# Kernel tuning notes

Measured on AMD Instinct MI355X. Metric: run time of the kernel, lower is better.

## Reference

```python
import jax, jax.numpy as jnp
import numpy as np

RES = 32  # voxel grid resolution per axis (cfg.MODEL.NEURAL_POINTS.VOXEL_RES)


def upsample_ac(x, s):
    """Bilinear upsample with align_corners=True. x: [B,C,h,w] -> [B,C,h*s,w*s]."""
    if s == 1:
        return x
    B, C, h, w = x.shape
    H, W = h * s, w * s
    ys = jnp.arange(H, dtype=x.dtype) * ((h - 1) / (H - 1))
    xs = jnp.arange(W, dtype=x.dtype) * ((w - 1) / (W - 1))
    y0 = jnp.floor(ys).astype(jnp.int32)
    x0 = jnp.floor(xs).astype(jnp.int32)
    y1 = jnp.minimum(y0 + 1, h - 1)
    x1 = jnp.minimum(x0 + 1, w - 1)
    wy = (ys - y0.astype(x.dtype))[:, None]  # [H,1]
    wx = (xs - x0.astype(x.dtype))[None, :]  # [1,W]
    top = x[:, :, y0, :]
    bot = x[:, :, y1, :]
    a = top[..., x0]; b = top[..., x1]; c = bot[..., x0]; d = bot[..., x1]
    return (a * (1 - wx) + b * wx) * (1 - wy) + (c * (1 - wx) + d * wx) * wy


def vox_closest(pos):
    """construct_vox_points_closest: per occupied voxel, index of point closest to
    the voxel's point centroid. pos: [N,3] -> [RES^3] int32 indices."""
    N = pos.shape[0]
    Vn = RES ** 3
    mn = pos.min(0)
    mx = pos.max(0)
    vsz = (mx - mn) / RES  # obtain_voxel_size_based_grid_res
    coord = jnp.clip(jnp.floor((pos - mn) / vsz).astype(jnp.int32), 0, RES - 1)
    vid = (coord[:, 0] * RES + coord[:, 1]) * RES + coord[:, 2]  # [N]
    cnt = jax.ops.segment_sum(jnp.ones((N,), pos.dtype), vid, Vn)
    cen = jax.ops.segment_sum(pos, vid, Vn) / jnp.maximum(cnt, 1.0)[:, None]
    d = jnp.sum((pos - cen[vid]) ** 2, axis=-1)  # [N] dist^2 to own-voxel centroid
    dmin = jax.ops.segment_min(d, vid, Vn)
    cand = jnp.where(d <= dmin[vid], jnp.arange(N, dtype=jnp.int32), N)
    midx = jax.ops.segment_min(cand, vid, Vn)
    return jnp.where(midx >= N, 0, midx)  # guard (rare) empty voxels


def reference(rgb, f1, f2, f3, points_pos, points_dir, W1, b1, W2, b2, points_mask):
    V, _, H, W = rgb.shape
    N = V * H * W
    C = 59
    # valid_index = where(points_mask == 1) (mask is all ones -> identity gather)
    valid = jnp.nonzero(points_mask[0] == 1, size=N, fill_value=0)[0]
    pos = points_pos[0, valid]          # [N,3]
    pdir = points_dir[0, valid]         # [N,3]
    # project_point_feats: upsample each pyramid level to full res, concat channels
    ups = [upsample_ac(rgb, 1), upsample_ac(f1, 2), upsample_ac(f2, 4), upsample_ac(f3, 8)]
    pif = jnp.concatenate(ups, axis=1)                       # [V,59,H,W]
    pif = jnp.transpose(pif, (0, 2, 3, 1)).reshape(N, C)     # [N,59]
    color = jax.lax.stop_gradient(jnp.transpose(rgb, (0, 2, 3, 1)).reshape(N, 3))
    pif = pif[valid]
    color = color[valid]
    emb = jnp.concatenate([pif, pdir], axis=-1)              # [N,62]
    midx = vox_closest(pos)                                  # [32768]
    sel_emb = emb[midx]
    sel_pos = pos[midx]
    sel_color = color[midx]
    sel_dir = pdir[midx]
    # point_mlp (premlp_init): 62 -> 256 -> 256
    h = jax.nn.relu(sel_emb @ W1 + b1)
    points_embedding = h @ W2 + b2
    return points_embedding, sel_pos, sel_color, sel_dir


def setup_inputs() -> dict:
    key = jax.random.key(0)
    ks = jax.random.split(key, 10)
    V, H, W = 8, 240, 320
    N = V * H * W
    return {
        "rgb": jax.random.uniform(ks[0], (V, 3, H, W), jnp.float32),
        "f1": jax.random.normal(ks[1], (V, 8, H // 2, W // 2), jnp.float32),
        "f2": jax.random.normal(ks[2], (V, 16, H // 4, W // 4), jnp.float32),
        "f3": jax.random.normal(ks[3], (V, 32, H // 8, W // 8), jnp.float32),
        "points_pos": jax.random.uniform(ks[4], (1, N, 3), jnp.float32),
        "points_dir": jax.random.normal(ks[5], (1, N, 3), jnp.float32),
        "W1": jax.random.normal(ks[6], (62, 256), jnp.float32) * 0.05,
        "b1": jnp.zeros((256,), jnp.float32),
        "W2": jax.random.normal(ks[7], (256, 256), jnp.float32) * 0.05,
        "b2": jnp.zeros((256,), jnp.float32),
        "points_mask": jnp.ones((1, N), jnp.int32),
    }
```

## Files before the change

kernel.cpp:

```cpp
#include <hip/hip_runtime.h>
#include <hip/hip_bf16.h>
#include <limits.h>
#include <stddef.h>

#define NPTS   614400
#define RESV   32
#define NVOX   (RESV*RESV*RESV)
#define IMG_H  240
#define IMG_W  320
#define IMG_HW (IMG_H*IMG_W)
#define INF    __builtin_inff()
#define CAP    64
#define SPILLCAP 4096

typedef __attribute__((ext_vector_type(8))) short short8;
typedef __attribute__((ext_vector_type(4))) short s16x4;
typedef __attribute__((ext_vector_type(4))) float f32x4;
typedef float f32x4u __attribute__((ext_vector_type(4), aligned(4)));

__device__ __forceinline__ float fadd_(float a, float b){
#pragma clang fp contract(off)
  return a + b;
}
__device__ __forceinline__ float fsub_(float a, float b){
#pragma clang fp contract(off)
  return a - b;
}
__device__ __forceinline__ float fmul_(float a, float b){
#pragma clang fp contract(off)
  return a * b;
}
__device__ __forceinline__ float fdiv_(float a, float b){
#pragma clang fp contract(off)
  return a / b;
}

__device__ __forceinline__ short f2bf(float x){
  __hip_bfloat16 h = __float2bfloat16(x);
  return *reinterpret_cast<short*>(&h);
}

__global__ void k_prep(int* __restrict__ cnt, int* __restrict__ spillcnt,
                       const float* __restrict__ W1, const float* __restrict__ W2,
                       short* __restrict__ W1t, short* __restrict__ W2t,
                       const float* __restrict__ pos,
                       f32x4* __restrict__ pmin, f32x4* __restrict__ pmax,
                       const float* __restrict__ f1, const float* __restrict__ f2,
                       const float* __restrict__ f3,
                       float* __restrict__ f1t, float* __restrict__ f2t,
                       float* __restrict__ f3t, int tposed){
  int gid = blockIdx.x*blockDim.x + threadIdx.x;
  int stride = gridDim.x*blockDim.x;
  if (gid < NVOX) cnt[gid] = 0;
  if (gid == 0) *spillcnt = 0;
  if (gid < 256*64){
    int n = gid >> 6, k = gid & 63;
    W1t[gid] = (k < 62) ? f2bf(W1[k*256 + n]) : (short)0;
  } else if (gid < 256*64 + 256*256){
    int j = gid - 256*64;
    int n = j >> 8, k = j & 255;
    W2t[j] = f2bf(W2[k*256 + n]);
  }

  if (tposed){
    for (int p = gid; p < 8*19200; p += stride){
      int img = p / 19200, pix = p - img*19200;
      const float* s = f1 + (size_t)img*8*19200 + pix;
      float r[8];
      #pragma unroll
      for (int c = 0; c < 8; c++) r[c] = s[(size_t)c*19200];
      float* d = f1t + (size_t)p*8;
      *(f32x4*)&d[0] = (f32x4){r[0],r[1],r[2],r[3]};
      *(f32x4*)&d[4] = (f32x4){r[4],r[5],r[6],r[7]};
    }
    for (int p = gid; p < 8*4800; p += stride){
      int img = p / 4800, pix = p - img*4800;
      const float* s = f2 + (size_t)img*16*4800 + pix;
      float* d = f2t + (size_t)p*16;
      #pragma unroll
      for (int cq = 0; cq < 4; cq++){
        f32x4 v = { s[(size_t)(4*cq+0)*4800], s[(size_t)(4*cq+1)*4800],
                    s[(size_t)(4*cq+2)*4800], s[(size_t)(4*cq+3)*4800] };
        *(f32x4*)&d[4*cq] = v;
      }
    }
    for (int p = gid; p < 8*1200; p += stride){
      int img = p / 1200, pix = p - img*1200;
      const float* s = f3 + (size_t)img*32*1200 + pix;
      float* d = f3t + (size_t)p*32;
      #pragma unroll
      for (int cq = 0; cq < 8; cq++){
        f32x4 v = { s[(size_t)(4*cq+0)*1200], s[(size_t)(4*cq+1)*1200],
                    s[(size_t)(4*cq+2)*1200], s[(size_t)(4*cq+3)*1200] };
        *(f32x4*)&d[4*cq] = v;
      }
    }
  }

  const f32x4* p4 = (const f32x4*)pos;
  float mn[3] = {  INF,  INF,  INF };
  float mx[3] = { -INF, -INF, -INF };
  for (int t = gid; t < NPTS/4; t += stride){
    f32x4 a = p4[3*t+0], b = p4[3*t+1], c = p4[3*t+2];
    mn[0] = fminf(mn[0], fminf(fminf(a.x, a.w), fminf(b.z, c.y)));
    mx[0] = fmaxf(mx[0], fmaxf(fmaxf(a.x, a.w), fmaxf(b.z, c.y)));
    mn[1] = fminf(mn[1], fminf(fminf(a.y, b.x), fminf(b.w, c.z)));
    mx[1] = fmaxf(mx[1], fmaxf(fmaxf(a.y, b.x), fmaxf(b.w, c.z)));
    mn[2] = fminf(mn[2], fminf(fminf(a.z, b.y), fminf(c.x, c.w)));
    mx[2] = fmaxf(mx[2], fmaxf(fmaxf(a.z, b.y), fmaxf(c.x, c.w)));
  }
  #pragma unroll
  for (int off = 32; off >= 1; off >>= 1){
    #pragma unroll
    for (int c = 0; c < 3; c++){
      mn[c] = fminf(mn[c], __shfl_down(mn[c], off, 64));
      mx[c] = fmaxf(mx[c], __shfl_down(mx[c], off, 64));
    }
  }
  __shared__ float smn[4][3], smx[4][3];
  int lane = threadIdx.x & 63, w = threadIdx.x >> 6;
  if (lane == 0){
    #pragma unroll
    for (int c = 0; c < 3; c++){ smn[w][c] = mn[c]; smx[w][c] = mx[c]; }
  }
  __syncthreads();
  if (threadIdx.x == 0){
    f32x4 a, b;
    a.x = fminf(fminf(smn[0][0], smn[1][0]), fminf(smn[2][0], smn[3][0]));
    a.y = fminf(fminf(smn[0][1], smn[1][1]), fminf(smn[2][1], smn[3][1]));
    a.z = fminf(fminf(smn[0][2], smn[1][2]), fminf(smn[2][2], smn[3][2]));
    a.w = 0.f;
    b.x = fmaxf(fmaxf(smx[0][0], smx[1][0]), fmaxf(smx[2][0], smx[3][0]));
    b.y = fmaxf(fmaxf(smx[0][1], smx[1][1]), fmaxf(smx[2][1], smx[3][1]));
    b.z = fmaxf(fmaxf(smx[0][2], smx[1][2]), fmaxf(smx[2][2], smx[3][2]));
    b.w = 0.f;
    pmin[blockIdx.x] = a;
    pmax[blockIdx.x] = b;
  }
}

__device__ __forceinline__ void reduce_minmax(const f32x4* __restrict__ pmin,
                                              const f32x4* __restrict__ pmax,
                                              float mn[3], float vsz[3]){
  int t = threadIdx.x;
  f32x4 a = pmin[t], b = pmin[t+256];
  f32x4 c = pmax[t], d = pmax[t+256];
  float lmn[3] = { fminf(a.x,b.x), fminf(a.y,b.y), fminf(a.z,b.z) };
  float lmx[3] = { fmaxf(c.x,d.x), fmaxf(c.y,d.y), fmaxf(c.z,d.z) };
  #pragma unroll
  for (int off = 32; off >= 1; off >>= 1){
    #pragma unroll
    for (int k = 0; k < 3; k++){
      lmn[k] = fminf(lmn[k], __shfl_xor(lmn[k], off, 64));
      lmx[k] = fmaxf(lmx[k], __shfl_xor(lmx[k], off, 64));
    }
  }
  __shared__ float smn[4][3], smx[4][3];
  int lane = t & 63, w = t >> 6;
  if (lane == 0){
    #pragma unroll
    for (int k = 0; k < 3; k++){ smn[w][k] = lmn[k]; smx[w][k] = lmx[k]; }
  }
  __syncthreads();
  #pragma unroll
  for (int k = 0; k < 3; k++){
    mn[k] = fminf(fminf(smn[0][k], smn[1][k]), fminf(smn[2][k], smn[3][k]));
    float mx = fmaxf(fmaxf(smx[0][k], smx[1][k]), fmaxf(smx[2][k], smx[3][k]));
    vsz[k] = fdiv_(fsub_(mx, mn[k]), 32.0f);
  }
}

__global__ void k_scatter(const float* __restrict__ pos,
                          const f32x4* __restrict__ pmin, const f32x4* __restrict__ pmax,
                          int* __restrict__ cnt, int* __restrict__ slots,
                          int* __restrict__ spillcnt, int2* __restrict__ spill){
  float mn[3], vsz[3];
  reduce_minmax(pmin, pmax, mn, vsz);

  int t = blockIdx.x*blockDim.x + threadIdx.x;
  const f32x4* p4 = (const f32x4*)pos;
  f32x4 a = p4[3*t+0], b = p4[3*t+1], c = p4[3*t+2];
  float X[4] = {a.x, a.w, b.z, c.y};
  float Y[4] = {a.y, b.x, b.w, c.z};
  float Z[4] = {a.z, b.y, c.x, c.w};
  #pragma unroll
  for (int j = 0; j < 4; j++){
    int i = 4*t + j;
    float P[3] = {X[j], Y[j], Z[j]};
    int v = 0;
    #pragma unroll
    for (int k = 0; k < 3; k++){
      float tt = fdiv_(fsub_(P[k], mn[k]), vsz[k]);
      int cc = (int)floorf(tt);
      cc = min(max(cc, 0), RESV-1);
      v = v*RESV + cc;
    }
    int p = atomicAdd(&cnt[v], 1);
    if (p < CAP){
      slots[v*CAP + p] = i;
    } else {
      int sp = atomicAdd(spillcnt, 1);
      if (sp < SPILLCAP){ int2 e; e.x = v; e.y = i; spill[sp] = e; }
    }
  }
}

__launch_bounds__(256)
__global__ void k_voxfull(const int* __restrict__ cnt, const int* __restrict__ slots,
                          const int* __restrict__ spillcnt, const int2* __restrict__ spill,
                          const float* __restrict__ pos,
                          const float* __restrict__ pdir, const float* __restrict__ rgb,
                          const float* __restrict__ f1, const float* __restrict__ f2,
                          const float* __restrict__ f3,
                          const float* __restrict__ f1t, const float* __restrict__ f2t,
                          const float* __restrict__ f3t, int tposed,
                          float* __restrict__ selpos, float* __restrict__ selcol,
                          float* __restrict__ seldir, short* __restrict__ emb){
  int lane = threadIdx.x & 63;
  int v = blockIdx.x*4 + (threadIdx.x >> 6);
  int n = cnt[v];
  int m = 0;
  unsigned long long ball = 0;
  float px = 0.f, py = 0.f, pz = 0.f;

  if (n > CAP){
    if (lane == 0){
      int sc = min(*spillcnt, SPILLCAP);
      float sx = 0.f, sy = 0.f, sz = 0.f; int last = -1;
      for (int i = 0; i < n; i++){
        int best = INT_MAX;
        for (int j = 0; j < CAP; j++){
          int id = slots[v*CAP + j];
          if (id > last && id < best) best = id;
        }
        for (int j = 0; j < sc; j++){
          int2 e = spill[j];
          if (e.x == v && e.y > last && e.y < best) best = e.y;
        }
        sx = fadd_(sx, pos[3*best+0]);
        sy = fadd_(sy, pos[3*best+1]);
        sz = fadd_(sz, pos[3*best+2]);
        last = best;
      }
      float cf = (float)n;
      float cx = fdiv_(sx, cf), cy = fdiv_(sy, cf), cz = fdiv_(sz, cf);
      float dmin = INF; int mm = 0;
      for (int j = 0; j < CAP + sc; j++){
        int id; int ok = 1;
        if (j < CAP) id = slots[v*CAP + j];
        else { int2 e = spill[j-CAP]; ok = (e.x == v); id = e.y; }
        if (!ok) continue;
        float dx = fsub_(pos[3*id+0], cx);
        float dy = fsub_(pos[3*id+1], cy);
        float dz = fsub_(pos[3*id+2], cz);
        float d  = fadd_(fadd_(fmul_(dx,dx), fmul_(dy,dy)), fmul_(dz,dz));
        if (d < dmin || (d == dmin && id < mm)){ dmin = d; mm = id; }
      }
      m = mm;
    }
    m = __shfl(m, 0, 64);
  } else {
    int key = INT_MAX;
    float gx = 0.f, gy = 0.f, gz = 0.f;
    if (lane < n){
      key = slots[v*CAP + lane];
      if (key < NPTS-1){
        f32x4u q = *(const f32x4u*)&pos[3*key];
        gx = q.x; gy = q.y; gz = q.z;
      } else {
        gx = pos[3*key+0]; gy = pos[3*key+1]; gz = pos[3*key+2];
      }
    }
    int src = lane;
    #pragma unroll
    for (int k = 2; k <= 64; k <<= 1){
      #pragma unroll
      for (int j = k >> 1; j >= 1; j >>= 1){
        int ok = __shfl_xor(key, j, 64);
        int os = __shfl_xor(src, j, 64);
        bool up    = ((lane & k) == 0);
        bool lower = ((lane & j) == 0);
        bool sw = (lower == up) ? (ok < key) : (ok > key);
        if (sw){ key = ok; src = os; }
      }
    }
    px = __shfl(gx, src, 64);
    py = __shfl(gy, src, 64);
    pz = __shfl(gz, src, 64);

    float sx = 0.f, sy = 0.f, sz = 0.f;
    for (int i = 0; i < n; i++){
      sx = fadd_(sx, __shfl(px, i, 64));
      sy = fadd_(sy, __shfl(py, i, 64));
      sz = fadd_(sz, __shfl(pz, i, 64));
    }
    float cf = fmaxf((float)n, 1.0f);
    float cx = fdiv_(sx, cf), cy = fdiv_(sy, cf), cz = fdiv_(sz, cf);

    float bd = INF; int bi = 0;
    if (lane < n){
      float dx = fsub_(px, cx), dy = fsub_(py, cy), dz = fsub_(pz, cz);
      bd = fadd_(fadd_(fmul_(dx,dx), fmul_(dy,dy)), fmul_(dz,dz));
      bi = key;
    }
    #pragma unroll
    for (int off = 32; off >= 1; off >>= 1){
      float od = __shfl_xor(bd, off, 64);
      int   oi = __shfl_xor(bi, off, 64);
      if (od < bd || (od == bd && oi < bi)){ bd = od; bi = oi; }
    }
    m = bi;
    ball = __ballot(lane < n && key == m);
  }

  float wx_ = 0.f, wy_ = 0.f, wz_ = 0.f;
  if (ball){
    int wl = (int)(__ffsll((long long)ball) - 1);
    wx_ = __shfl(px, wl, 64);
    wy_ = __shfl(py, wl, 64);
    wz_ = __shfl(pz, wl, 64);
  }

  int img = m / IMG_HW;
  int rem = m - img*IMG_HW;
  int y = rem / IMG_W;
  int x = rem - y*IMG_W;
  int ch = lane;
  float val;
  if (ch < 3){
    val = rgb[((img*3 + ch)*IMG_H + y)*IMG_W + x];
    selcol[3*v+ch] = val;
    float sp = ball ? ((ch == 0) ? wx_ : (ch == 1) ? wy_ : wz_) : pos[3*m+ch];
    selpos[3*v+ch] = sp;
  } else if (ch < 59){
    int lvl = (ch >= 27) ? 2 : ((ch >= 11) ? 1 : 0);
    int c   = ch - ((lvl == 0) ? 3 : ((lvl == 1) ? 11 : 27));
    int C   = 8 << lvl;
    int h   = 120 >> lvl, w = 160 >> lvl;
    float ry = (lvl == 0) ? (119.0f/239.0f) : ((lvl == 1) ? (59.0f/239.0f) : (29.0f/239.0f));
    float rx = (lvl == 0) ? (159.0f/319.0f) : ((lvl == 1) ? (79.0f/319.0f) : (39.0f/319.0f));
    float ys = (float)y * ry;
    float xs = (float)x * rx;
    int y0 = (int)floorf(ys);
    int x0 = (int)floorf(xs);
    int y1 = min(y0+1, h-1);
    int x1 = min(x0+1, w-1);
    float wy = ys - (float)y0;
    float wx = xs - (float)x0;
    float aa, bb, cc, dd;
    if (tposed){
      const float* ft = (lvl == 0) ? f1t : ((lvl == 1) ? f2t : f3t);
      const float* base = ft + (size_t)(img*h*w)*C + c;
      aa = base[(y0*w + x0)*C];
      bb = base[(y0*w + x1)*C];
      cc = base[(y1*w + x0)*C];
      dd = base[(y1*w + x1)*C];
    } else {
      const float* f = (lvl == 0) ? f1 : ((lvl == 1) ? f2 : f3);
      const float* plane = f + ((size_t)img*C + c)*(size_t)(h*w);
      aa = plane[y0*w + x0];
      bb = plane[y0*w + x1];
      cc = plane[y1*w + x0];
      dd = plane[y1*w + x1];
    }
    val = (aa*(1.f-wx) + bb*wx)*(1.f-wy) + (cc*(1.f-wx) + dd*wx)*wy;
  } else if (ch < 62){
    val = pdir[3*m + (ch-59)];
    seldir[3*v+(ch-59)] = val;
  } else {
    val = 0.f;
  }
  emb[(size_t)v*64 + ch] = f2bf(val);
}

#define MLP_BLOCKS 512
#define MLP_TILES  (NVOX/16/MLP_BLOCKS)
__launch_bounds__(256, 2)
__global__ void k_mlp(const short* __restrict__ emb, const short* __restrict__ W1t,
                      const float* __restrict__ b1f, const short* __restrict__ W2t,
                      const float* __restrict__ b2f, float* __restrict__ out){
  __shared__ short Hs[16][264];
  int t    = threadIdx.x;
  int lane = t & 63;
  int wv   = t >> 6;
  int m    = lane & 15;
  int q    = lane >> 4;

  short8 w1f[4][2], w2f[4][8];
  float  b1r[4][4], b2r[4];
  #pragma unroll
  for (int nt = 0; nt < 4; nt++){
    int n = wv*64 + nt*16 + m;
    #pragma unroll
    for (int kq = 0; kq < 2; kq++)
      w1f[nt][kq] = *(const short8*)&W1t[(size_t)n*64 + kq*32 + q*8];
    #pragma unroll
    for (int kq = 0; kq < 8; kq++)
      w2f[nt][kq] = *(const short8*)&W2t[(size_t)n*256 + kq*32 + q*8];
    #pragma unroll
    for (int i = 0; i < 4; i++)
      b1r[nt][i] = b1f[wv*64 + nt*16 + q*4 + i];
    b2r[nt] = b2f[n];
  }

  for (int tt = 0; tt < MLP_TILES; tt++){
    int row0 = (blockIdx.x*MLP_TILES + tt)*16;

    short8 ef0 = *(const short8*)&emb[(size_t)(row0 + m)*64 + q*8];
    short8 ef1 = *(const short8*)&emb[(size_t)(row0 + m)*64 + 32 + q*8];

    #pragma unroll
    for (int nt = 0; nt < 4; nt++){
      f32x4 c = {0.f, 0.f, 0.f, 0.f};
      c = __builtin_amdgcn_mfma_f32_16x16x32_bf16(w1f[nt][0], ef0, c, 0, 0, 0);
      c = __builtin_amdgcn_mfma_f32_16x16x32_bf16(w1f[nt][1], ef1, c, 0, 0, 0);
      s16x4 hv;
      #pragma unroll
      for (int i = 0; i < 4; i++)
        hv[i] = f2bf(fmaxf(c[i] + b1r[nt][i], 0.f));
      *(s16x4*)&Hs[m][wv*64 + nt*16 + q*4] = hv;
    }
    __syncthreads();

    f32x4 acc[4] = {{0,0,0,0},{0,0,0,0},{0,0,0,0},{0,0,0,0}};
    #pragma unroll
    for (int kq = 0; kq < 8; kq++){
      short8 af = *(const short8*)&Hs[m][kq*32 + q*8];
      #pragma unroll
      for (int nt = 0; nt < 4; nt++)
        acc[nt] = __builtin_amdgcn_mfma_f32_16x16x32_bf16(af, w2f[nt][kq], acc[nt], 0, 0, 0);
    }
    __syncthreads();

    #pragma unroll
    for (int nt = 0; nt < 4; nt++){
      int n = wv*64 + nt*16 + m;
      #pragma unroll
      for (int i = 0; i < 4; i++)
        out[(size_t)(row0 + q*4 + i)*256 + n] = acc[nt][i] + b2r[nt];
    }
  }
}

extern "C" void kernel_launch(void* const* d_in, const int* in_sizes, int n_in,
                              void* d_out, int out_size, void* d_ws, size_t ws_size,
                              hipStream_t stream){
  const float* rgb  = (const float*)d_in[0];
  const float* f1   = (const float*)d_in[1];
  const float* f2   = (const float*)d_in[2];
  const float* f3   = (const float*)d_in[3];
  const float* pos  = (const float*)d_in[4];
  const float* pdir = (const float*)d_in[5];
  const float* W1   = (const float*)d_in[6];
  const float* b1   = (const float*)d_in[7];
  const float* W2   = (const float*)d_in[8];
  const float* b2   = (const float*)d_in[9];

  float* out      = (float*)d_out;
  float* out_emb  = out;
  float* out_pos  = out + (size_t)NVOX*256;
  float* out_col  = out_pos + (size_t)NVOX*3;
  float* out_dir  = out_col + (size_t)NVOX*3;

  char* w = (char*)d_ws;
  int*   spillcnt = (int*)w;       w += 64;
  f32x4* pmin     = (f32x4*)w;     w += (size_t)512*16;
  f32x4* pmax     = (f32x4*)w;     w += (size_t)512*16;
  int*   cnt      = (int*)w;       w += (size_t)NVOX*4;
  short* W1t      = (short*)w;     w += (size_t)256*64*2;
  short* W2t      = (short*)w;     w += (size_t)256*256*2;
  short* emb      = (short*)w;     w += (size_t)NVOX*64*2;
  int2*  spill    = (int2*)w;      w += (size_t)SPILLCAP*8;
  int*   slots    = (int*)w;       w += (size_t)NVOX*CAP*4;
  float* f1t      = (float*)w;     w += (size_t)8*19200*8*4;
  float* f2t      = (float*)w;     w += (size_t)8*4800*16*4;
  float* f3t      = (float*)w;     w += (size_t)8*1200*32*4;

  int tposed = ((size_t)(w - (char*)d_ws) <= ws_size) ? 1 : 0;

  k_prep    <<<512,    256, 0, stream>>>(cnt, spillcnt, W1, W2, W1t, W2t, pos, pmin, pmax,
                                         f1, f2, f3, f1t, f2t, f3t, tposed);
  k_scatter <<<NPTS/1024, 256, 0, stream>>>(pos, pmin, pmax, cnt, slots, spillcnt, spill);
  k_voxfull <<<NVOX/4, 256, 0, stream>>>(cnt, slots, spillcnt, spill,
                                         pos, pdir, rgb, f1, f2, f3,
                                         f1t, f2t, f3t, tposed,
                                         out_pos, out_col, out_dir, emb);
  k_mlp     <<<MLP_BLOCKS, 256, 0, stream>>>(emb, W1t, b1, W2t, b2, out_emb);
}
```

Before: 202.6 us.

## Store point coordinates with slot indices and rank-sort keys via LDS

The scatter kernel now writes each point's xyz and index into a per-voxel slot buffer (up to 32 entries), so the voxel kernel reads the positions with one coalesced load instead of gathering them from pos by index. The 64-lane bitonic shuffle sort is replaced by a rank count over keys staged in shared memory, followed by a scatter of positions into sorted order in LDS. Centroid accumulation then reads from LDS instead of using shuffles. This costs an extra 16-byte scattered write per point in the scatter kernel and extra workspace, and it only takes effect when the workspace is large enough.

```diff
diff --git a/kernel.cpp b/kernel.cpp
--- a/kernel.cpp
+++ b/kernel.cpp
@@ -11,6 +11,7 @@
 #define IMG_HW (IMG_H*IMG_W)
 #define INF    __builtin_inff()
 #define CAP    64
+#define CAPP   32
 #define SPILLCAP 4096
 
 typedef __attribute__((ext_vector_type(8))) short short8;
@@ -173,7 +174,8 @@
 __global__ void k_scatter(const float* __restrict__ pos,
                           const f32x4* __restrict__ pmin, const f32x4* __restrict__ pmax,
                           int* __restrict__ cnt, int* __restrict__ slots,
-                          int* __restrict__ spillcnt, int2* __restrict__ spill){
+                          int* __restrict__ spillcnt, int2* __restrict__ spill,
+                          f32x4* __restrict__ slotpos, int haspp){
   float mn[3], vsz[3];
   reduce_minmax(pmin, pmax, mn, vsz);
 
@@ -196,6 +198,10 @@
       v = v*RESV + cc;
     }
     int p = atomicAdd(&cnt[v], 1);
+    if (haspp && p < CAPP){
+      f32x4 e = { P[0], P[1], P[2], __int_as_float(i) };
+      slotpos[(size_t)v*CAPP + p] = e;
+    }
     if (p < CAP){
       slots[v*CAP + p] = i;
     } else {
@@ -208,6 +214,7 @@
 __launch_bounds__(256)
 __global__ void k_voxfull(const int* __restrict__ cnt, const int* __restrict__ slots,
                           const int* __restrict__ spillcnt, const int2* __restrict__ spill,
+                          const f32x4* __restrict__ slotpos, int haspp,
                           const float* __restrict__ pos,
                           const float* __restrict__ pdir, const float* __restrict__ rgb,
                           const float* __restrict__ f1, const float* __restrict__ f2,
@@ -216,9 +223,16 @@
                           const float* __restrict__ f3t, int tposed,
                           float* __restrict__ selpos, float* __restrict__ selcol,
                           float* __restrict__ seldir, short* __restrict__ emb){
+  __shared__ __align__(16) int skey[4][64];
+  __shared__ f32x4 sposl[4][64];
   int lane = threadIdx.x & 63;
-  int v = blockIdx.x*4 + (threadIdx.x >> 6);
+  int wv   = threadIdx.x >> 6;
+  int v = blockIdx.x*4 + wv;
+
+  f32x4 q = {0.f, 0.f, 0.f, 0.f};
+  if (haspp) q = slotpos[(size_t)v*CAPP + (lane & (CAPP-1))];
   int n = cnt[v];
+
   int m = 0;
   unsigned long long ball = 0;
   float px = 0.f, py = 0.f, pz = 0.f;
@@ -261,38 +275,46 @@
     m = __shfl(m, 0, 64);
   } else {
     int key = INT_MAX;
-    float gx = 0.f, gy = 0.f, gz = 0.f;
+    if (haspp && n <= CAPP){
+      if (lane < n){
+        px = q.x; py = q.y; pz = q.z;
+        key = __float_as_int(q.w);
+      }
+    } else {
+      if (lane < n){
+        key = slots[v*CAP + lane];
+        if (key < NPTS-1){
+          f32x4u qq = *(const f32x4u*)&pos[3*key];
+          px = qq.x; py = qq.y; pz = qq.z;
+        } else {
+          px = pos[3*key+0]; py = pos[3*key+1]; pz = pos[3*key+2];
+        }
+      }
+    }
+
+    skey[wv][lane] = key;
+    __builtin_amdgcn_wave_barrier();
+    int r = 0;
+    {
+      int nq = (n + 3) >> 2;
+      const int4* k4 = (const int4*)&skey[wv][0];
+      for (int j = 0; j < nq; j++){
+        int4 kk = k4[j];
+        r += (kk.x < key) + (kk.y < key) + (kk.z < key) + (kk.w < key);
+      }
+    }
     if (lane < n){
-      key = slots[v*CAP + lane];
-      if (key < NPTS-1){
-        f32x4u q = *(const f32x4u*)&pos[3*key];
-        gx = q.x; gy = q.y; gz = q.z;
-      } else {
-        gx = pos[3*key+0]; gy = pos[3*key+1]; gz = pos[3*key+2];
-      }
-    }
-    int src = lane;
-    #pragma unroll
-    for (int k = 2; k <= 64; k <<= 1){
-      #pragma unroll
-      for (int j = k >> 1; j >= 1; j >>= 1){
-        int ok = __shfl_xor(key, j, 64);
-        int os = __shfl_xor(src, j, 64);
-        bool up    = ((lane & k) == 0);
-        bool lower = ((lane & j) == 0);
-        bool sw = (lower == up) ? (ok < key) : (ok > key);
-        if (sw){ key = ok; src = os; }
-      }
-    }
-    px = __shfl(gx, src, 64);
-    py = __shfl(gy, src, 64);
-    pz = __shfl(gz, src, 64);
+      f32x4 e = { px, py, pz, 0.f };
+      sposl[wv][r] = e;
+    }
+    __builtin_amdgcn_wave_barrier();
 
     float sx = 0.f, sy = 0.f, sz = 0.f;
     for (int i = 0; i < n; i++){
-      sx = fadd_(sx, __shfl(px, i, 64));
-      sy = fadd_(sy, __shfl(py, i, 64));
-      sz = fadd_(sz, __shfl(pz, i, 64));
+      f32x4 pp = sposl[wv][i];
+      sx = fadd_(sx, pp.x);
+      sy = fadd_(sy, pp.y);
+      sz = fadd_(sz, pp.z);
     }
     float cf = fmaxf((float)n, 1.0f);
     float cx = fdiv_(sx, cf), cy = fdiv_(sy, cf), cz = fdiv_(sz, cf);
@@ -475,13 +497,15 @@
   float* f1t      = (float*)w;     w += (size_t)8*19200*8*4;
   float* f2t      = (float*)w;     w += (size_t)8*4800*16*4;
   float* f3t      = (float*)w;     w += (size_t)8*1200*32*4;
-
   int tposed = ((size_t)(w - (char*)d_ws) <= ws_size) ? 1 : 0;
+  f32x4* slotpos  = (f32x4*)w;     w += (size_t)NVOX*CAPP*16;
+  int haspp = ((size_t)(w - (char*)d_ws) <= ws_size) ? 1 : 0;
 
   k_prep    <<<512,    256, 0, stream>>>(cnt, spillcnt, W1, W2, W1t, W2t, pos, pmin, pmax,
                                          f1, f2, f3, f1t, f2t, f3t, tposed);
-  k_scatter <<<NPTS/1024, 256, 0, stream>>>(pos, pmin, pmax, cnt, slots, spillcnt, spill);
-  k_voxfull <<<NVOX/4, 256, 0, stream>>>(cnt, slots, spillcnt, spill,
+  k_scatter <<<NPTS/1024, 256, 0, stream>>>(pos, pmin, pmax, cnt, slots, spillcnt, spill,
+                                            slotpos, haspp);
+  k_voxfull <<<NVOX/4, 256, 0, stream>>>(cnt, slots, spillcnt, spill, slotpos, haspp,
                                          pos, pdir, rgb, f1, f2, f3,
                                          f1t, f2t, f3t, tposed,
                                          out_pos, out_col, out_dir, emb);
```

Measured after the change: 192.5 us. 1.05x faster.
